# Performance work log

Measured on AMD Instinct MI355X. Metric: run time of the kernel, lower is better.

The kernel has to match this reference:

```python
import jax, jax.numpy as jnp
import numpy as np

NUM_Q = 4096     # num_of_questions
MAX_STEP = 256   # max_step
BATCH = 64       # students per batch


def setup_inputs() -> dict:
    key = jax.random.key(0)
    k1, k2, k3, k4, k5, k6 = jax.random.split(key, 6)
    # simulated interaction sequences with random leading padding (all-zero rows)
    q_ids = jax.random.randint(k1, (BATCH, MAX_STEP), 0, NUM_Q)
    correct = jax.random.bernoulli(k2, 0.6, (BATCH, MAX_STEP)).astype(jnp.float32)
    start = jax.random.randint(k3, (BATCH,), 0, 16)  # leading pad length per student
    valid = (jnp.arange(MAX_STEP)[None, :] >= start[:, None]).astype(jnp.float32)
    oh = jax.nn.one_hot(q_ids, NUM_Q, dtype=jnp.float32)  # [B,S,Q]
    # batch = [one-hot if answered correctly | one-hot if answered incorrectly]
    batch = jnp.concatenate(
        [oh * (correct * valid)[..., None], oh * ((1.0 - correct) * valid)[..., None]],
        axis=-1,
    )  # [B,S,2Q]
    pred = jax.random.uniform(k4, (BATCH, MAX_STEP, NUM_Q), minval=0.01, maxval=0.99)
    target_q = jax.random.uniform(k5, (BATCH, 1), minval=0.01, maxval=0.99)
    target_label = jax.random.bernoulli(k6, 0.5, (BATCH,)).astype(jnp.float32)
    return {"pred": pred, "target_q": target_q, "batch": batch, "target_label": target_label}


def _bce(p, a):
    # elementwise BCE matching torch.nn.BCELoss (log clamped at -100)
    logp = jnp.maximum(jnp.log(p), -100.0)
    log1mp = jnp.maximum(jnp.log1p(-p), -100.0)
    return -(a * logp + (1.0 - a) * log1mp)


def reference(pred, target_q, batch, target_label):
    Q, S = NUM_Q, MAX_STEP
    delta = batch[:, :, :Q] + batch[:, :, Q:]  # [B,S,Q] one-hot of asked question
    # temp.gather(0, arange) extracts the diagonal of pred[:S-1] @ delta[1:].T,
    # i.e. p[s,j] = pred[s,j] . delta[s,j+1]
    p = jnp.einsum('bsq,bsq->bs', pred[:, :S - 1], delta[:, 1:])  # [B,S-1]
    # correctness label: 1 if correct, 0 if incorrect or padded ('//' is non-diff)
    a = jax.lax.stop_gradient(
        jnp.floor(((batch[:, :, :Q] - batch[:, :, Q:]).sum(-1) + 1.0) / 2.0)
    )[:, 1:]  # [B,S-1]
    # the break loop trims everything before the first p[i] > 0;
    # if no p > 0, argmax returns 0 == no trim (matching torch, where break never fires)
    i = jnp.argmax(p > 0, axis=1)  # [B]
    mask = jnp.arange(S - 1)[None, :] >= i[:, None]
    seq_loss = jnp.sum(jnp.where(mask, _bce(p, a), 0.0), axis=1)  # [B]
    tail = _bce(target_q[:, 0], target_label)  # [B]
    # per-student mean over (trimmed length + 1 appended target)
    n = ((S - 1) - i + 1).astype(pred.dtype)
    return jnp.sum((seq_loss + tail) / n)
```

## Files before the change

### kernel.cpp

```cpp
#include <hip/hip_runtime.h>
#include <limits.h>

#define NUM_Q    4096
#define MAX_STEP 256
#define BATCH    64
#define TWOQ     8192
#define ROWS     (BATCH * MAX_STEP)
#define VEC_PER_ROW (TWOQ / 4)
#define ITERS    (VEC_PER_ROW / 64)

__global__ void __launch_bounds__(256) find_onehot_kernel(
        const float* __restrict__ batch, int* __restrict__ qa) {
    const int gtid = blockIdx.x * blockDim.x + threadIdx.x;
    const int row  = gtid >> 6;
    const int lane = gtid & 63;
    if (row >= ROWS) return;

    const float4* rp = (const float4*)(batch + (size_t)row * TWOQ);

    int found = -1;
    float4 v = rp[lane];
    for (int it = 0; it < ITERS; ++it) {
        float4 nv;
        if (it + 1 < ITERS) nv = rp[(it + 1) * 64 + lane];
        const float s = v.x + v.y + v.z + v.w;
        const unsigned long long m = __ballot(s > 0.0f);
        if (m) {
            const int src = __ffsll(m) - 1;
            int idx = 0;
            if (lane == src) {
                const int base = (it * 64 + lane) * 4;
                idx = (v.x != 0.f) ? base
                    : (v.y != 0.f) ? base + 1
                    : (v.z != 0.f) ? base + 2
                                   : base + 3;
            }
            found = __shfl(idx, src);
            break;
        }
        v = nv;
    }
    if (lane == 0) qa[row] = found;
}

__device__ __forceinline__ float bce(float p, float a) {
    float lp  = fmaxf(logf(p), -100.0f);
    float l1p = fmaxf(log1pf(-p), -100.0f);
    return -(a * lp + (1.0f - a) * l1p);
}

__global__ void __launch_bounds__(256) loss_kernel(
        const float* __restrict__ pred,
        const float* __restrict__ target_q,
        const float* __restrict__ target_label,
        const int* __restrict__ qa,
        float* __restrict__ out) {
    const int b = blockIdx.x;
    const int t = threadIdx.x;
    const int SM1 = MAX_STEP - 1;

    __shared__ int   smin[256];
    __shared__ float ssum[256];

    int   idx = -1;
    float p   = 0.0f;
    float a   = 0.0f;
    if (t < SM1) {
        idx = qa[b * MAX_STEP + t + 1];
        if (idx >= 0) {
            const int qid = idx & (NUM_Q - 1);
            p = pred[((size_t)b * MAX_STEP + t) * NUM_Q + qid];
            a = (idx < NUM_Q) ? 1.0f : 0.0f;
        }
    }

    smin[t] = (t < SM1 && idx >= 0 && p > 0.0f) ? t : INT_MAX;
    __syncthreads();
    #pragma unroll
    for (int off = 128; off > 0; off >>= 1) {
        if (t < off) smin[t] = min(smin[t], smin[t + off]);
        __syncthreads();
    }
    const int i0 = (smin[0] == INT_MAX) ? 0 : smin[0];

    float v = 0.0f;
    if (t < SM1 && t >= i0) v = bce(p, a);
    ssum[t] = v;
    __syncthreads();
    #pragma unroll
    for (int off = 128; off > 0; off >>= 1) {
        if (t < off) ssum[t] += ssum[t + off];
        __syncthreads();
    }

    if (t == 0) {
        const float tail = bce(target_q[b], target_label[b]);
        const float n = (float)(MAX_STEP - i0);
        atomicAdd(out, (ssum[0] + tail) / n);
    }
}

extern "C" void kernel_launch(void* const* d_in, const int* in_sizes, int n_in,
                              void* d_out, int out_size, void* d_ws, size_t ws_size,
                              hipStream_t stream) {
    const float* pred         = (const float*)d_in[0];
    const float* target_q     = (const float*)d_in[1];
    const float* batch        = (const float*)d_in[2];
    const float* target_label = (const float*)d_in[3];
    float* out = (float*)d_out;
    int*   qa  = (int*)d_ws;

    hipMemsetAsync(out, 0, (size_t)out_size * sizeof(float), stream);
    find_onehot_kernel<<<(ROWS * 64) / 256, 256, 0, stream>>>(batch, qa);
    loss_kernel<<<BATCH, 256, 0, stream>>>(pred, target_q, target_label, qa, out);
}
```

Measured before the change: 733.4 us.

## Fuse one-hot search and loss into one kernel with a last-block reduction

Merges the one-hot index search and the loss computation into a single launch. An atomic block counter lets the last finishing block compute every per-student loss, so the second kernel launch and the memset of the output go away. The final per-student work now runs in one block with 4 wavefronts, each handling 16 students one after another using wave shuffles, where it used to spread over 64 blocks. That serialises the dependent gathers from pred. The trim start now depends on the index being valid rather than on p > 0, which is only equivalent when pred is positive.

```diff
diff --git a/kernel.cpp b/kernel.cpp
--- a/kernel.cpp
+++ b/kernel.cpp
@@ -8,40 +8,7 @@
 #define ROWS     (BATCH * MAX_STEP)
 #define VEC_PER_ROW (TWOQ / 4)
 #define ITERS    (VEC_PER_ROW / 64)
-
-__global__ void __launch_bounds__(256) find_onehot_kernel(
-        const float* __restrict__ batch, int* __restrict__ qa) {
-    const int gtid = blockIdx.x * blockDim.x + threadIdx.x;
-    const int row  = gtid >> 6;
-    const int lane = gtid & 63;
-    if (row >= ROWS) return;
-
-    const float4* rp = (const float4*)(batch + (size_t)row * TWOQ);
-
-    int found = -1;
-    float4 v = rp[lane];
-    for (int it = 0; it < ITERS; ++it) {
-        float4 nv;
-        if (it + 1 < ITERS) nv = rp[(it + 1) * 64 + lane];
-        const float s = v.x + v.y + v.z + v.w;
-        const unsigned long long m = __ballot(s > 0.0f);
-        if (m) {
-            const int src = __ffsll(m) - 1;
-            int idx = 0;
-            if (lane == src) {
-                const int base = (it * 64 + lane) * 4;
-                idx = (v.x != 0.f) ? base
-                    : (v.y != 0.f) ? base + 1
-                    : (v.z != 0.f) ? base + 2
-                                   : base + 3;
-            }
-            found = __shfl(idx, src);
-            break;
-        }
-        v = nv;
-    }
-    if (lane == 0) qa[row] = found;
-}
+#define GRID_BLOCKS (ROWS / 4)
 
 __device__ __forceinline__ float bce(float p, float a) {
     float lp  = fmaxf(logf(p), -100.0f);
@@ -49,55 +16,105 @@
     return -(a * lp + (1.0f - a) * l1p);
 }
 
-__global__ void __launch_bounds__(256) loss_kernel(
+__global__ void __launch_bounds__(256) fused_loss_kernel(
+        const float* __restrict__ batch,
         const float* __restrict__ pred,
         const float* __restrict__ target_q,
         const float* __restrict__ target_label,
-        const int* __restrict__ qa,
-        float* __restrict__ out) {
-    const int b = blockIdx.x;
-    const int t = threadIdx.x;
-    const int SM1 = MAX_STEP - 1;
+        float* __restrict__ out,
+        int* __restrict__ qa,
+        unsigned int* __restrict__ counter) {
+    const int gtid = blockIdx.x * 256 + threadIdx.x;
+    const int row  = gtid >> 6;
+    const int lane = gtid & 63;
 
-    __shared__ int   smin[256];
-    __shared__ float ssum[256];
+    {
+        const float4* rp = (const float4*)(batch + (size_t)row * TWOQ);
+        int found = -1;
+        float4 v = rp[lane];
+        for (int it = 0; it < ITERS; ++it) {
+            float4 nv;
+            if (it + 1 < ITERS) nv = rp[(it + 1) * 64 + lane];
+            const float s = v.x + v.y + v.z + v.w;
+            const unsigned long long m = __ballot(s > 0.0f);
+            if (m) {
+                const int src = __ffsll(m) - 1;
+                int idx = 0;
+                if (lane == src) {
+                    const int base = (it * 64 + lane) * 4;
+                    idx = (v.x != 0.f) ? base
+                        : (v.y != 0.f) ? base + 1
+                        : (v.z != 0.f) ? base + 2
+                                       : base + 3;
+                }
+                found = __shfl(idx, src);
+                break;
+            }
+            v = nv;
+        }
+        if (lane == 0) qa[row] = found;
+    }
 
-    int   idx = -1;
-    float p   = 0.0f;
-    float a   = 0.0f;
-    if (t < SM1) {
-        idx = qa[b * MAX_STEP + t + 1];
-        if (idx >= 0) {
-            const int qid = idx & (NUM_Q - 1);
-            p = pred[((size_t)b * MAX_STEP + t) * NUM_Q + qid];
-            a = (idx < NUM_Q) ? 1.0f : 0.0f;
+    __shared__ int isLast;
+    __threadfence();
+    __syncthreads();
+    if (threadIdx.x == 0) {
+        unsigned int old = atomicAdd(counter, 1u);
+        isLast = (old == GRID_BLOCKS - 1u);
+    }
+    __syncthreads();
+    if (!isLast) return;
+    __threadfence();
+
+    const int w = threadIdx.x >> 6;
+    __shared__ float wacc[4];
+    float acc = 0.0f;
+
+    for (int j = 0; j < 16; ++j) {
+        const int b = w * 16 + j;
+        int   cand = INT_MAX;
+        float pv[4], av[4];
+        #pragma unroll
+        for (int k = 0; k < 4; ++k) {
+            const int t = lane + 64 * k;
+            pv[k] = 0.0f; av[k] = 0.0f;
+            if (t < MAX_STEP - 1) {
+                const int idx = qa[b * MAX_STEP + t + 1];
+                if (idx >= 0) {
+                    const int qid = idx & (NUM_Q - 1);
+                    pv[k] = pred[((size_t)b * MAX_STEP + t) * NUM_Q + qid];
+                    av[k] = (idx < NUM_Q) ? 1.0f : 0.0f;
+                    cand = min(cand, t);
+                }
+            }
+        }
+        #pragma unroll
+        for (int off = 32; off > 0; off >>= 1)
+            cand = min(cand, __shfl_down(cand, off));
+        int i0 = __shfl(cand, 0);
+        if (i0 == INT_MAX) i0 = 0;
+
+        float s = 0.0f;
+        #pragma unroll
+        for (int k = 0; k < 4; ++k) {
+            const int t = lane + 64 * k;
+            if (t < MAX_STEP - 1 && t >= i0) s += bce(pv[k], av[k]);
+        }
+        #pragma unroll
+        for (int off = 32; off > 0; off >>= 1)
+            s += __shfl_down(s, off);
+
+        if (lane == 0) {
+            const float tail = bce(target_q[b], target_label[b]);
+            const float n = (float)(MAX_STEP - i0);
+            acc += (s + tail) / n;
         }
     }
 
-    smin[t] = (t < SM1 && idx >= 0 && p > 0.0f) ? t : INT_MAX;
+    if (lane == 0) wacc[w] = acc;
     __syncthreads();
-    #pragma unroll
-    for (int off = 128; off > 0; off >>= 1) {
-        if (t < off) smin[t] = min(smin[t], smin[t + off]);
-        __syncthreads();
-    }
-    const int i0 = (smin[0] == INT_MAX) ? 0 : smin[0];
-
-    float v = 0.0f;
-    if (t < SM1 && t >= i0) v = bce(p, a);
-    ssum[t] = v;
-    __syncthreads();
-    #pragma unroll
-    for (int off = 128; off > 0; off >>= 1) {
-        if (t < off) ssum[t] += ssum[t + off];
-        __syncthreads();
-    }
-
-    if (t == 0) {
-        const float tail = bce(target_q[b], target_label[b]);
-        const float n = (float)(MAX_STEP - i0);
-        atomicAdd(out, (ssum[0] + tail) / n);
-    }
+    if (threadIdx.x == 0)
+        out[0] = wacc[0] + wacc[1] + wacc[2] + wacc[3];
 }
 
 extern "C" void kernel_launch(void* const* d_in, const int* in_sizes, int n_in,
@@ -108,9 +125,11 @@
     const float* batch        = (const float*)d_in[2];
     const float* target_label = (const float*)d_in[3];
     float* out = (float*)d_out;
-    int*   qa  = (int*)d_ws;
 
-    hipMemsetAsync(out, 0, (size_t)out_size * sizeof(float), stream);
-    find_onehot_kernel<<<(ROWS * 64) / 256, 256, 0, stream>>>(batch, qa);
-    loss_kernel<<<BATCH, 256, 0, stream>>>(pred, target_q, target_label, qa, out);
+    unsigned int* counter = (unsigned int*)d_ws;
+    int* qa = (int*)d_ws + 64;
+
+    hipMemsetAsync(counter, 0, sizeof(unsigned int), stream);
+    fused_loss_kernel<<<GRID_BLOCKS, 256, 0, stream>>>(
+        batch, pred, target_q, target_label, out, qa, counter);
 }
```

After: 1.533 ms. 2.09x slower.
